# Kernel tuning notes

Hardware: AMD Instinct MI355X
Metric: run time of the kernel (lower is better)

## Reference

```python
import jax, jax.numpy as jnp
import numpy as np

N = 50000
E = 800000
D_IN = 128
D_HID = 256


def setup_inputs() -> dict:
    key = jax.random.key(0)
    ks = jax.random.split(key, 9)
    x = jax.random.normal(ks[0], (N, D_IN), dtype=jnp.float32)
    edge_index = jax.random.randint(ks[1], (2, E), 0, N, dtype=jnp.int64)
    edge_weight = jax.random.uniform(ks[2], (E,), dtype=jnp.float32)
    # GCNConv params (lin: y = x @ W.T, plus bias added after aggregation)
    W1 = jax.random.normal(ks[3], (D_HID, D_IN), dtype=jnp.float32) / np.sqrt(D_IN)
    b1 = jnp.zeros((D_HID,), dtype=jnp.float32)
    W2 = jax.random.normal(ks[4], (D_IN, D_HID), dtype=jnp.float32) / np.sqrt(D_HID)
    b2 = jnp.zeros((D_IN,), dtype=jnp.float32)
    gamma = jnp.ones((D_IN,), dtype=jnp.float32)
    beta = jnp.zeros((D_IN,), dtype=jnp.float32)
    return {"x": x, "edge_index": edge_index, "edge_weight": edge_weight,
            "W1": W1, "b1": b1, "W2": W2, "b2": b2,
            "gamma": gamma, "beta": beta}


def _gcn_norm(edge_index, edge_weight, n_nodes):
    # add self loops with weight 1.0 (PyG gcn_norm default)
    loop = jnp.arange(n_nodes, dtype=edge_index.dtype)
    src = jnp.concatenate([edge_index[0], loop])
    dst = jnp.concatenate([edge_index[1], loop])
    w = jnp.concatenate([edge_weight, jnp.ones((n_nodes,), edge_weight.dtype)])
    # symmetric normalization: deg over target index
    deg = jax.ops.segment_sum(w, dst, num_segments=n_nodes)
    dinv = jnp.where(deg > 0, jax.lax.rsqrt(deg), 0.0)
    norm = dinv[src] * w * dinv[dst]
    return src, dst, norm


def _gcn_conv(x, src, dst, norm, W, b, n_nodes):
    h = x @ W.T                                    # [N, out]
    msg = h[src] * norm[:, None]                   # gather + scale [E+N, out]
    out = jax.ops.segment_sum(msg, dst, num_segments=n_nodes)
    return out + b


def reference(x, edge_index, edge_weight, W1, b1, W2, b2, gamma, beta):
    n_nodes = x.shape[0]
    src, dst, norm = _gcn_norm(edge_index, edge_weight, n_nodes)
    h = _gcn_conv(x, src, dst, norm, W1, b1, n_nodes)
    h = jax.nn.relu(h)
    h = _gcn_conv(h, src, dst, norm, W2, b2, n_nodes)
    # LayerNorm over last dim
    mu = jnp.mean(h, axis=-1, keepdims=True)
    var = jnp.mean(jnp.square(h - mu), axis=-1, keepdims=True)
    h = (h - mu) * jax.lax.rsqrt(var + 1e-5) * gamma + beta
    return h
```

## Files before the change

### kernel.cpp

```cpp
#include <hip/hip_runtime.h>

typedef unsigned short ushort_t;
typedef __attribute__((ext_vector_type(8))) short short8;
typedef __attribute__((ext_vector_type(4))) float float4v;

#define MAXDEG 48

__device__ inline float b2f(ushort_t u) {
    unsigned x = ((unsigned)u) << 16;
    return __builtin_bit_cast(float, x);
}
__device__ inline ushort_t f2b(float f) {
    unsigned x = __builtin_bit_cast(unsigned, f);
    unsigned r = (x + 0x7fffu + ((x >> 16) & 1u)) >> 16;
    return (ushort_t)r;
}

__device__ inline void load_edge(const int* __restrict__ ei, int e, int E,
                                 int& s, int& d) {
    int ec = min(e, E - 1);
    int2 c64 = ((const int2*)ei)[ec];
    unsigned long long m = __ballot(c64.y != 0);
    if (m != 0ull) {
        s = ei[ec];
        d = ei[(size_t)E + ec];
    } else {
        s = c64.x;
        d = ((const int2*)ei)[(size_t)E + ec].x;
    }
}


__global__ __launch_bounds__(256) void k_mega(const int* __restrict__ ei,
                                              const float* __restrict__ w,
                                              const float* __restrict__ x,
                                              const float* __restrict__ W1,
                                              const float* __restrict__ W2,
                                              unsigned* packed,
                                              unsigned* __restrict__ edata,
                                              ushort_t* __restrict__ xb,
                                              ushort_t* __restrict__ W1b,
                                              ushort_t* __restrict__ W2b,
                                              int E, int Nn, int gE, int gX) {
    int b = blockIdx.x;
    bool isEdge;
    int widx;
    if (3 * gE <= (int)gridDim.x) {
        if (b < 3 * gE) {
            if (b % 3 == 0) { isEdge = true;  widx = b / 3; }
            else            { isEdge = false; widx = b - b / 3 - 1; }
        } else {
            isEdge = false; widx = b - gE;
        }
    } else {
        isEdge = b < gE;
        widx = isEdge ? b : b - gE;
    }

    if (isEdge) {
        int e = widx * 256 + threadIdx.x;
        int s, d;
        load_edge(ei, e, E, s, d);
        if (e < E) {
            if ((unsigned)s < (unsigned)Nn && (unsigned)d < (unsigned)Nn) {
                float wv = w[e];
                unsigned fx = (unsigned)(wv * 65536.0f + 0.5f);
                unsigned old = atomicAdd(packed + d, (1u << 22) | fx);
                int r = (int)(old >> 22);
                if (r < MAXDEG) {
                    unsigned wq = (unsigned)(wv * 32768.0f + 0.5f);
                    wq = min(wq, 32767u);
                    edata[(size_t)d * MAXDEG + r] = ((unsigned)s << 15) | wq;
                }
            }
        }
    } else if (widx < gX) {
        int i = widx * 256 + threadIdx.x;
        if (i < Nn * 32) {
            float4v v = ((const float4v*)x)[i];
            ushort4 o;
            o.x = f2b(v[0]); o.y = f2b(v[1]); o.z = f2b(v[2]); o.w = f2b(v[3]);
            ((ushort4*)xb)[i] = o;
        }
    } else {
        int i = (widx - gX) * 256 + threadIdx.x;
        if (i < 32768) W1b[i] = f2b(W1[i]);
        else if (i < 65536) W2b[i - 32768] = f2b(W2[i - 32768]);
    }
}


__global__ __launch_bounds__(256) void k_dinv(const unsigned* __restrict__ packed,
                                              float* __restrict__ dinv, int Nn) {
    int i = blockIdx.x * 256 + threadIdx.x;
    if (i < Nn) {
        float wsum = (float)(packed[i] & 0x3FFFFFu) * (1.0f / 65536.0f);
        dinv[i] = rsqrtf(1.0f + wsum);
    }
}


__device__ inline void agg_edges(const ushort_t* __restrict__ src,
                                 const unsigned* __restrict__ ed, int n,
                                 const float* __restrict__ dinv,
                                 int hl, int p, float* a) {
    int i = 0;
    for (; i + 15 < n; i += 16) {
        unsigned e2[8];
#pragma unroll
        for (int j = 0; j < 8; ++j) e2[j] = ed[i + p + 2 * j];
        ushort4 q[8];
        float nw[8];
#pragma unroll
        for (int j = 0; j < 8; ++j) {
            int sN = (int)(e2[j] >> 15);
            q[j] = ((const ushort4*)(src + (size_t)sN * 128))[hl];
            nw[j] = dinv[sN] * (float)(e2[j] & 0x7FFFu) * (1.0f / 32768.0f);
        }
#pragma unroll
        for (int j = 0; j < 8; ++j) {
            a[0] += b2f(q[j].x) * nw[j]; a[1] += b2f(q[j].y) * nw[j];
            a[2] += b2f(q[j].z) * nw[j]; a[3] += b2f(q[j].w) * nw[j];
        }
    }
    for (; i + 7 < n; i += 8) {
        unsigned e2[4];
#pragma unroll
        for (int j = 0; j < 4; ++j) e2[j] = ed[i + p + 2 * j];
        ushort4 q[4];
        float nw[4];
#pragma unroll
        for (int j = 0; j < 4; ++j) {
            int sN = (int)(e2[j] >> 15);
            q[j] = ((const ushort4*)(src + (size_t)sN * 128))[hl];
            nw[j] = dinv[sN] * (float)(e2[j] & 0x7FFFu) * (1.0f / 32768.0f);
        }
#pragma unroll
        for (int j = 0; j < 4; ++j) {
            a[0] += b2f(q[j].x) * nw[j]; a[1] += b2f(q[j].y) * nw[j];
            a[2] += b2f(q[j].z) * nw[j]; a[3] += b2f(q[j].w) * nw[j];
        }
    }
    for (; i < n; i += 2) {
        int idx = i + p;
        int ic = min(idx, n - 1);
        unsigned e2 = ed[ic];
        int sN = (int)(e2 >> 15);
        float nw = (idx < n)
                       ? dinv[sN] * (float)(e2 & 0x7FFFu) * (1.0f / 32768.0f)
                       : 0.f;
        ushort4 q = ((const ushort4*)(src + (size_t)sN * 128))[hl];
        a[0] += b2f(q.x) * nw; a[1] += b2f(q.y) * nw;
        a[2] += b2f(q.z) * nw; a[3] += b2f(q.w) * nw;
    }
}


__global__ __launch_bounds__(256) void k_agg1(const ushort_t* __restrict__ xb,
                                              const unsigned* __restrict__ packed,
                                              const unsigned* __restrict__ edata,
                                              const float* __restrict__ dinv,
                                              ushort_t* __restrict__ ax, int Nn) {
    int v = (blockIdx.x * blockDim.x + threadIdx.x) >> 6;
    int lane = threadIdx.x & 63;
    if (v >= Nn) return;
    int hl = lane & 31, p = lane >> 5;
    float dv = dinv[v];
    float a[4] = {0.f, 0.f, 0.f, 0.f};
    if (p == 0) {
        ushort4 pq = ((const ushort4*)(xb + (size_t)v * 128))[hl];
        a[0] = b2f(pq.x) * dv; a[1] = b2f(pq.y) * dv;
        a[2] = b2f(pq.z) * dv; a[3] = b2f(pq.w) * dv;
    }
    int n = min((int)(packed[v] >> 22), MAXDEG);
    agg_edges(xb, edata + (size_t)v * MAXDEG, n, dinv, hl, p, a);
#pragma unroll
    for (int j = 0; j < 4; ++j) {
        a[j] *= dv;
        a[j] += __shfl_xor(a[j], 32);
    }
    if (p == 0) {
        ushort4 o;
        o.x = f2b(a[0]); o.y = f2b(a[1]); o.z = f2b(a[2]); o.w = f2b(a[3]);
        ((ushort4*)(ax + (size_t)v * 128))[hl] = o;
    }
}


__global__ __launch_bounds__(256, 2) void k_gemm_fused(const ushort_t* __restrict__ ax,
                                                       const ushort_t* __restrict__ W1b,
                                                       const float* __restrict__ b1v,
                                                       const ushort_t* __restrict__ W2b,
                                                       ushort_t* __restrict__ h2, int Nn) {
    __shared__ ushort_t tile[64][264];
    int tid = threadIdx.x, wid = tid >> 6, lane = tid & 63;
    int m = lane & 15, q = lane >> 4;
    int blk = blockIdx.x * 64;

    short8 wf[4][4];
#pragma unroll
    for (int nt = 0; nt < 4; ++nt) {
        const ushort_t* wb = W1b + (size_t)(wid * 64 + nt * 16 + m) * 128 + q * 8;
#pragma unroll
        for (int kt = 0; kt < 4; ++kt) wf[nt][kt] = *(const short8*)(wb + kt * 32);
    }
    short8 af[4][4];
#pragma unroll
    for (int mi = 0; mi < 4; ++mi) {
        int arow = blk + mi * 16 + m;
        bool rv = arow < Nn;
        const ushort_t* ab = ax + (size_t)arow * 128 + q * 8;
#pragma unroll
        for (int kt = 0; kt < 4; ++kt)
            af[mi][kt] = rv ? *(const short8*)(ab + kt * 32) : (short8)0;
    }

    float4v acc1[4][4];
#pragma unroll
    for (int mi = 0; mi < 4; ++mi)
#pragma unroll
        for (int nt = 0; nt < 4; ++nt) acc1[mi][nt] = (float4v){0.f, 0.f, 0.f, 0.f};

#pragma unroll
    for (int kt = 0; kt < 4; ++kt)
#pragma unroll
        for (int mi = 0; mi < 4; ++mi)
#pragma unroll
            for (int nt = 0; nt < 4; ++nt)
                acc1[mi][nt] = __builtin_amdgcn_mfma_f32_16x16x32_bf16(
                    af[mi][kt], wf[nt][kt], acc1[mi][nt], 0, 0, 0);

#pragma unroll
    for (int nt = 0; nt < 4; ++nt) {
        int col = wid * 64 + nt * 16 + m;
        float bb = b1v[col];
#pragma unroll
        for (int mi = 0; mi < 4; ++mi) {
#pragma unroll
            for (int r = 0; r < 4; ++r) {
                float v = acc1[mi][nt][r] + bb;
                v = v > 0.f ? v : 0.f;
                tile[mi * 16 + q * 4 + r][col] = f2b(v);
            }
        }
    }
    __syncthreads();

    short8 w2f[2][8];
#pragma unroll
    for (int n2 = 0; n2 < 2; ++n2) {
        const ushort_t* wb = W2b + (size_t)(wid * 32 + n2 * 16 + m) * 256 + q * 8;
#pragma unroll
        for (int kt = 0; kt < 8; ++kt) w2f[n2][kt] = *(const short8*)(wb + kt * 32);
    }

    float4v acc2[4][2];
#pragma unroll
    for (int mi = 0; mi < 4; ++mi)
#pragma unroll
        for (int n2 = 0; n2 < 2; ++n2) acc2[mi][n2] = (float4v){0.f, 0.f, 0.f, 0.f};

#pragma unroll
    for (int kt = 0; kt < 8; ++kt) {
#pragma unroll
        for (int mi = 0; mi < 4; ++mi) {
            short8 a2 = *(const short8*)&tile[mi * 16 + m][kt * 32 + q * 8];
#pragma unroll
            for (int n2 = 0; n2 < 2; ++n2)
                acc2[mi][n2] = __builtin_amdgcn_mfma_f32_16x16x32_bf16(
                    a2, w2f[n2][kt], acc2[mi][n2], 0, 0, 0);
        }
    }

#pragma unroll
    for (int mi = 0; mi < 4; ++mi) {
#pragma unroll
        for (int n2 = 0; n2 < 2; ++n2) {
            int col = wid * 32 + n2 * 16 + m;
#pragma unroll
            for (int r = 0; r < 4; ++r) {
                int row = blk + mi * 16 + q * 4 + r;
                if (row < Nn) h2[(size_t)row * 128 + col] = f2b(acc2[mi][n2][r]);
            }
        }
    }
}


__global__ __launch_bounds__(256) void k_agg2_ln(const ushort_t* __restrict__ h2,
                                                 const unsigned* __restrict__ packed,
                                                 const unsigned* __restrict__ edata,
                                                 const float* __restrict__ dinv,
                                                 const float* __restrict__ b2v,
                                                 const float* __restrict__ gv,
                                                 const float* __restrict__ bev,
                                                 float* __restrict__ out, int Nn) {
    int v = (blockIdx.x * blockDim.x + threadIdx.x) >> 6;
    int lane = threadIdx.x & 63;
    if (v >= Nn) return;
    int hl = lane & 31, p = lane >> 5;
    float dv = dinv[v];
    float a[4] = {0.f, 0.f, 0.f, 0.f};
    if (p == 0) {
        ushort4 pq = ((const ushort4*)(h2 + (size_t)v * 128))[hl];
        a[0] = b2f(pq.x) * dv; a[1] = b2f(pq.y) * dv;
        a[2] = b2f(pq.z) * dv; a[3] = b2f(pq.w) * dv;
    }
    int n = min((int)(packed[v] >> 22), MAXDEG);
    agg_edges(h2, edata + (size_t)v * MAXDEG, n, dinv, hl, p, a);
#pragma unroll
    for (int j = 0; j < 4; ++j) {
        a[j] *= dv;
        a[j] += __shfl_xor(a[j], 32);
    }

    int d0 = hl * 4;
#pragma unroll
    for (int j = 0; j < 4; ++j) a[j] += b2v[d0 + j];

    float ssum = a[0] + a[1] + a[2] + a[3];
    float ssq = a[0] * a[0] + a[1] * a[1] + a[2] * a[2] + a[3] * a[3];
#pragma unroll
    for (int off = 1; off < 64; off <<= 1) {
        ssum += __shfl_xor(ssum, off);
        ssq += __shfl_xor(ssq, off);
    }
    float mu = ssum * (1.0f / 256.0f);
    float var = ssq * (1.0f / 256.0f) - mu * mu;
    float r = rsqrtf(var + 1e-5f);
    if (p == 0) {
        float4v o;
#pragma unroll
        for (int j = 0; j < 4; ++j)
            o[j] = (a[j] - mu) * r * gv[d0 + j] + bev[d0 + j];
        ((float4v*)(out + (size_t)v * 128))[hl] = o;
    }
}


extern "C" void kernel_launch(void* const* d_in, const int* in_sizes, int n_in,
                              void* d_out, int out_size, void* d_ws, size_t ws_size,
                              hipStream_t stream) {
    const float* x   = (const float*)d_in[0];
    const int*   ei  = (const int*)d_in[1];
    const float* ew  = (const float*)d_in[2];
    const float* W1  = (const float*)d_in[3];
    const float* b1v = (const float*)d_in[4];
    const float* W2  = (const float*)d_in[5];
    const float* b2v = (const float*)d_in[6];
    const float* gv  = (const float*)d_in[7];
    const float* bev = (const float*)d_in[8];
    float* out = (float*)d_out;

    const int Nn = in_sizes[0] / 128;
    const int E  = in_sizes[2];

    char* base = (char*)d_ws;
    size_t off = 0;
    auto alloc = [&](size_t bytes) {
        char* p = base + off;
        off = (off + bytes + 255) & ~(size_t)255;
        return p;
    };
    unsigned* packed = (unsigned*)alloc((size_t)Nn * 4);
    float*    dinv   = (float*)alloc((size_t)Nn * 4);
    unsigned* edata  = (unsigned*)alloc((size_t)Nn * MAXDEG * 4);
    ushort_t* xb     = (ushort_t*)alloc((size_t)Nn * 128 * 2);
    ushort_t* h2     = (ushort_t*)alloc((size_t)Nn * 128 * 2);
    ushort_t* W1b    = (ushort_t*)alloc(32768 * 2);
    ushort_t* W2b    = (ushort_t*)alloc(32768 * 2);
    ushort_t* ax     = (ushort_t*)d_out;
    (void)ws_size; (void)n_in; (void)out_size;

    int gE = (E + 255) / 256;
    int gX = (Nn * 32 + 255) / 256;
    int gW = (Nn + 3) / 4;
    int gG = (Nn + 63) / 64;
    int gD = (Nn + 255) / 256;

    hipMemsetAsync(packed, 0, (size_t)Nn * 4, stream);
    k_mega<<<gE + gX + 256, 256, 0, stream>>>(ei, ew, x, W1, W2, packed, edata,
                                              xb, W1b, W2b, E, Nn, gE, gX);
    k_dinv<<<gD, 256, 0, stream>>>(packed, dinv, Nn);
    k_agg1<<<gW, 256, 0, stream>>>(xb, packed, edata, dinv, ax, Nn);
    k_gemm_fused<<<gG, 256, 0, stream>>>(ax, W1b, b1v, W2b, h2, Nn);
    k_agg2_ln<<<gW, 256, 0, stream>>>(h2, packed, edata, dinv, b2v, gv, bev, out, Nn);
}
```

Baseline: 243.4 us.

## Map one half-wavefront per node in aggregation kernels, dropping edge split

The two aggregation kernels now assign 32 lanes per destination node instead of a full 64-lane wavefront that split the edge list across two halves. Each half-wave walks all edges in one masked loop of 8, so the cross-half shuffle reduction and the separate remainder loops go away, and the LayerNorm reduction shrinks to 32 lanes. This doubles nodes per wavefront and removes idle-lane work on writes. In exchange, each half-wave runs longer serial gather chains, padding to multiples of 8 adds wasted loads on low-degree nodes, and the two nodes sharing a wavefront can have different degrees and diverge.

```diff
diff --git a/kernel.cpp b/kernel.cpp
--- a/kernel.cpp
+++ b/kernel.cpp
@@ -103,55 +103,27 @@
 __device__ inline void agg_edges(const ushort_t* __restrict__ src,
                                  const unsigned* __restrict__ ed, int n,
                                  const float* __restrict__ dinv,
-                                 int hl, int p, float* a) {
-    int i = 0;
-    for (; i + 15 < n; i += 16) {
+                                 int hl, float* a) {
+    for (int i = 0; i < n; i += 8) {
         unsigned e2[8];
 #pragma unroll
-        for (int j = 0; j < 8; ++j) e2[j] = ed[i + p + 2 * j];
+        for (int j = 0; j < 8; ++j) e2[j] = ed[min(i + j, n - 1)];
         ushort4 q[8];
         float nw[8];
 #pragma unroll
         for (int j = 0; j < 8; ++j) {
             int sN = (int)(e2[j] >> 15);
             q[j] = ((const ushort4*)(src + (size_t)sN * 128))[hl];
-            nw[j] = dinv[sN] * (float)(e2[j] & 0x7FFFu) * (1.0f / 32768.0f);
+            float d = dinv[sN];
+            nw[j] = (i + j < n)
+                        ? d * (float)(e2[j] & 0x7FFFu) * (1.0f / 32768.0f)
+                        : 0.f;
         }
 #pragma unroll
         for (int j = 0; j < 8; ++j) {
             a[0] += b2f(q[j].x) * nw[j]; a[1] += b2f(q[j].y) * nw[j];
             a[2] += b2f(q[j].z) * nw[j]; a[3] += b2f(q[j].w) * nw[j];
         }
-    }
-    for (; i + 7 < n; i += 8) {
-        unsigned e2[4];
-#pragma unroll
-        for (int j = 0; j < 4; ++j) e2[j] = ed[i + p + 2 * j];
-        ushort4 q[4];
-        float nw[4];
-#pragma unroll
-        for (int j = 0; j < 4; ++j) {
-            int sN = (int)(e2[j] >> 15);
-            q[j] = ((const ushort4*)(src + (size_t)sN * 128))[hl];
-            nw[j] = dinv[sN] * (float)(e2[j] & 0x7FFFu) * (1.0f / 32768.0f);
-        }
-#pragma unroll
-        for (int j = 0; j < 4; ++j) {
-            a[0] += b2f(q[j].x) * nw[j]; a[1] += b2f(q[j].y) * nw[j];
-            a[2] += b2f(q[j].z) * nw[j]; a[3] += b2f(q[j].w) * nw[j];
-        }
-    }
-    for (; i < n; i += 2) {
-        int idx = i + p;
-        int ic = min(idx, n - 1);
-        unsigned e2 = ed[ic];
-        int sN = (int)(e2 >> 15);
-        float nw = (idx < n)
-                       ? dinv[sN] * (float)(e2 & 0x7FFFu) * (1.0f / 32768.0f)
-                       : 0.f;
-        ushort4 q = ((const ushort4*)(src + (size_t)sN * 128))[hl];
-        a[0] += b2f(q.x) * nw; a[1] += b2f(q.y) * nw;
-        a[2] += b2f(q.z) * nw; a[3] += b2f(q.w) * nw;
     }
 }
 
@@ -161,29 +133,18 @@
                                               const unsigned* __restrict__ edata,
                                               const float* __restrict__ dinv,
                                               ushort_t* __restrict__ ax, int Nn) {
-    int v = (blockIdx.x * blockDim.x + threadIdx.x) >> 6;
-    int lane = threadIdx.x & 63;
+    int v = (blockIdx.x * blockDim.x + threadIdx.x) >> 5;
+    int hl = threadIdx.x & 31;
     if (v >= Nn) return;
-    int hl = lane & 31, p = lane >> 5;
     float dv = dinv[v];
-    float a[4] = {0.f, 0.f, 0.f, 0.f};
-    if (p == 0) {
-        ushort4 pq = ((const ushort4*)(xb + (size_t)v * 128))[hl];
-        a[0] = b2f(pq.x) * dv; a[1] = b2f(pq.y) * dv;
-        a[2] = b2f(pq.z) * dv; a[3] = b2f(pq.w) * dv;
-    }
+    ushort4 pq = ((const ushort4*)(xb + (size_t)v * 128))[hl];
+    float a[4] = {b2f(pq.x) * dv, b2f(pq.y) * dv, b2f(pq.z) * dv, b2f(pq.w) * dv};
     int n = min((int)(packed[v] >> 22), MAXDEG);
-    agg_edges(xb, edata + (size_t)v * MAXDEG, n, dinv, hl, p, a);
-#pragma unroll
-    for (int j = 0; j < 4; ++j) {
-        a[j] *= dv;
-        a[j] += __shfl_xor(a[j], 32);
-    }
-    if (p == 0) {
-        ushort4 o;
-        o.x = f2b(a[0]); o.y = f2b(a[1]); o.z = f2b(a[2]); o.w = f2b(a[3]);
-        ((ushort4*)(ax + (size_t)v * 128))[hl] = o;
-    }
+    agg_edges(xb, edata + (size_t)v * MAXDEG, n, dinv, hl, a);
+    ushort4 o;
+    o.x = f2b(a[0] * dv); o.y = f2b(a[1] * dv);
+    o.z = f2b(a[2] * dv); o.w = f2b(a[3] * dv);
+    ((ushort4*)(ax + (size_t)v * 128))[hl] = o;
 }
 
 
@@ -295,46 +256,37 @@
                                                  const float* __restrict__ gv,
                                                  const float* __restrict__ bev,
                                                  float* __restrict__ out, int Nn) {
-    int v = (blockIdx.x * blockDim.x + threadIdx.x) >> 6;
-    int lane = threadIdx.x & 63;
+    int v = (blockIdx.x * blockDim.x + threadIdx.x) >> 5;
+    int hl = threadIdx.x & 31;
     if (v >= Nn) return;
-    int hl = lane & 31, p = lane >> 5;
     float dv = dinv[v];
-    float a[4] = {0.f, 0.f, 0.f, 0.f};
-    if (p == 0) {
-        ushort4 pq = ((const ushort4*)(h2 + (size_t)v * 128))[hl];
-        a[0] = b2f(pq.x) * dv; a[1] = b2f(pq.y) * dv;
-        a[2] = b2f(pq.z) * dv; a[3] = b2f(pq.w) * dv;
-    }
+    ushort4 pq = ((const ushort4*)(h2 + (size_t)v * 128))[hl];
+    float a[4] = {b2f(pq.x) * dv, b2f(pq.y) * dv, b2f(pq.z) * dv, b2f(pq.w) * dv};
     int n = min((int)(packed[v] >> 22), MAXDEG);
-    agg_edges(h2, edata + (size_t)v * MAXDEG, n, dinv, hl, p, a);
+    agg_edges(h2, edata + (size_t)v * MAXDEG, n, dinv, hl, a);
+
+    int d0 = hl * 4;
 #pragma unroll
     for (int j = 0; j < 4; ++j) {
         a[j] *= dv;
-        a[j] += __shfl_xor(a[j], 32);
-    }
-
-    int d0 = hl * 4;
-#pragma unroll
-    for (int j = 0; j < 4; ++j) a[j] += b2v[d0 + j];
+        a[j] += b2v[d0 + j];
+    }
 
     float ssum = a[0] + a[1] + a[2] + a[3];
     float ssq = a[0] * a[0] + a[1] * a[1] + a[2] * a[2] + a[3] * a[3];
 #pragma unroll
-    for (int off = 1; off < 64; off <<= 1) {
+    for (int off = 1; off < 32; off <<= 1) {
         ssum += __shfl_xor(ssum, off);
         ssq += __shfl_xor(ssq, off);
     }
-    float mu = ssum * (1.0f / 256.0f);
-    float var = ssq * (1.0f / 256.0f) - mu * mu;
+    float mu = ssum * (1.0f / 128.0f);
+    float var = ssq * (1.0f / 128.0f) - mu * mu;
     float r = rsqrtf(var + 1e-5f);
-    if (p == 0) {
-        float4v o;
-#pragma unroll
-        for (int j = 0; j < 4; ++j)
-            o[j] = (a[j] - mu) * r * gv[d0 + j] + bev[d0 + j];
-        ((float4v*)(out + (size_t)v * 128))[hl] = o;
-    }
+    float4v o;
+#pragma unroll
+    for (int j = 0; j < 4; ++j)
+        o[j] = (a[j] - mu) * r * gv[d0 + j] + bev[d0 + j];
+    ((float4v*)(out + (size_t)v * 128))[hl] = o;
 }
 
 
@@ -374,7 +326,7 @@
 
     int gE = (E + 255) / 256;
     int gX = (Nn * 32 + 255) / 256;
-    int gW = (Nn + 3) / 4;
+    int gW = (Nn + 7) / 8;
     int gG = (Nn + 63) / 64;
     int gD = (Nn + 255) / 256;
 
```

After: 241.7 us. About the same (-0.7%).
